# Optimization experiments

Measured on AMD Instinct MI355X. Metric: run time of the kernel, lower is better.

## Reference

```python
import jax, jax.numpy as jnp
import numpy as np
from jax.scipy.special import gammaln, logsumexp

S, K, O, H = 64, 16, 32, 30   # state_dim, act_dim, obs_dim, horizon
T, N = 200, 512               # seq len, batch
EPS = 1e-6
LOG2PI = float(np.log(2.0 * np.pi))
NUM_PARAMS = S * O * 2 + K * S * S + S + S + 1


def setup_inputs() -> dict:
    key = jax.random.key(0)
    k1, k2, k3 = jax.random.split(key, 3)
    o = jax.random.normal(k1, (T, N, O), dtype=jnp.float32)
    a = jax.random.randint(k2, (T, N), 0, K)
    theta = jax.random.normal(k3, (N, NUM_PARAMS), dtype=jnp.float32)
    return {"o": o, "a": a, "theta": theta}


def _transform_params(theta):
    sizes = [S * O * 2, K * S * S, S, S, 1]
    idx = np.cumsum(sizes)[:-1]
    tA, tB, tC, tD, ttau = jnp.split(theta, idx, axis=-1)
    A_mean, A_lv = jnp.split(tA, 2, axis=-1)
    A_mean = A_mean.reshape(-1, S, O)
    A_std = jax.nn.softplus(A_lv.reshape(-1, S, O)) + EPS  # rectify
    B = jax.nn.softmax(tB.reshape(-1, K, S, S), axis=-1)
    C = jax.nn.softmax(tC.reshape(-1, 1, S), axis=-1)
    D = jax.nn.softmax(tD.reshape(-1, S), axis=-1)
    tau = jax.nn.sigmoid(ttau) * (2.0 * H) + 1.0  # [N,1]
    return A_mean, A_std, B, C, D, tau


def reference(o, a, theta):
    A_mean, A_std, B, C, D, tau = _transform_params(theta)

    # --- negative expected free energy reward: r[n,k,i] ---
    ent = jnp.sum(0.5 + 0.5 * LOG2PI + jnp.log(A_std), axis=-1)          # Normal entropy, [N,S]
    kl = jnp.sum(B * (jnp.log(B + EPS) - jnp.log(C[:, None] + EPS)), -1)  # KL(B || C), [N,K,S]
    eh = jnp.einsum('nkij,nj->nki', B, ent)
    r = -kl - eh

    # --- finite-horizon value iteration: q [H,N,K,S] ---
    def vi_step(qt, _):
        v = logsumexp(qt, axis=-2)                    # [N,S]
        qn = r + jnp.einsum('nkij,nj->nki', B, v)
        return qn, qn
    _, q_rest = jax.lax.scan(vi_step, r, None, length=H - 1)
    q = jnp.concatenate([r[None], q_rest], axis=0)

    # --- truncated poisson horizon weights: pdf [N,H] ---
    hh = jnp.arange(H, dtype=jnp.float32)
    logp_h = hh[None, :] * jnp.log(tau) - tau - gammaln(hh + 1.0)[None, :]
    pdf = jnp.exp(logp_h)
    pdf = pdf / jnp.sum(pdf, axis=-1, keepdims=True)

    batch_idx = jnp.arange(N)

    def time_step(b, inp):
        o_t, a_t = inp
        # policy from current belief
        qb = jnp.einsum('ni,hnki->hnk', b, q)
        pi_h = jax.nn.softmax(qb, axis=-1)
        pi_t = jnp.einsum('hnk,nh->nk', pi_h, pdf)
        # belief update
        B_a = B[batch_idx, a_t]                       # [N,S,S]
        s = jnp.einsum('nij,ni->nj', B_a, b)
        logp_s = jnp.log(s + EPS)
        lp = -0.5 * ((o_t[:, None, :] - A_mean) / A_std) ** 2 \
             - jnp.log(A_std) - 0.5 * LOG2PI          # [N,S,O]
        joint = logp_s + jnp.sum(lp, axis=-1)         # [N,S]
        b_next = jax.nn.softmax(joint, axis=-1)
        logp_o = logsumexp(joint, axis=-1)
        return b_next, (pi_t, b, logp_o)

    _, (pi, b_seq, logp_o) = jax.lax.scan(time_step, D, (o, a))
    return pi, b_seq, logp_o
```

## Files before the change

### kernel.cpp

```cpp
#include <hip/hip_runtime.h>
#include <hip/hip_bf16.h>
#include <math.h>

#define SDIM 64
#define KDIM 16
#define ODIM 32
#define HDIM 30
#define TDIM 200
#define NDIM 512
#define NP 69761
#define EPSV 1e-6f
#define LOG2PIF 1.8378770664093453f

__device__ __forceinline__ float softplusf(float x) {
    return (x > 0.f) ? x + log1pf(expf(-x)) : log1pf(expf(x));
}
__device__ __forceinline__ float wave_max64(float v) {
#pragma unroll
    for (int off = 32; off; off >>= 1) v = fmaxf(v, __shfl_xor(v, off, 64));
    return v;
}
__device__ __forceinline__ float wave_sum64(float v) {
#pragma unroll
    for (int off = 32; off; off >>= 1) v += __shfl_xor(v, off, 64);
    return v;
}
__device__ __forceinline__ void bar_lds() {
    asm volatile("s_waitcnt lgkmcnt(0)\n\ts_barrier" ::: "memory");
}

__global__ __launch_bounds__(256) void transform_kernel(
    const float* __restrict__ theta, float* __restrict__ invstd,
    float* __restrict__ c0, float* __restrict__ ent,
    float* __restrict__ logC, float* __restrict__ Dws,
    float* __restrict__ pdfws)
{
    __shared__ float ls[SDIM * 33];
    const int n = blockIdx.x, tid = threadIdx.x;
    const float* thn = theta + (size_t)n * NP;

    for (int idx = tid; idx < SDIM * ODIM; idx += 256) {
        float x = thn[2048 + idx];
        float sp = softplusf(x) + EPSV;
        invstd[(size_t)n * SDIM * ODIM + idx] = 1.f / sp;
        int s = idx >> 5, oo = idx & 31;
        ls[s * 33 + oo] = logf(sp);
    }
    __syncthreads();

    const int wave = tid >> 6, lane = tid & 63;
    if (wave == 0) {
        float sum = 0.f;
#pragma unroll
        for (int oo = 0; oo < ODIM; ++oo) sum += ls[lane * 33 + oo];
        c0[n * SDIM + lane]  = -sum - 16.f * LOG2PIF;
        ent[n * SDIM + lane] =  sum + 32.f * (0.5f + 0.5f * LOG2PIF);
    } else if (wave == 1) {
        float x = thn[69632 + lane];
        float m = wave_max64(x);
        float e = expf(x - m);
        float ssum = wave_sum64(e);
        logC[n * SDIM + lane] = logf(e / ssum + EPSV);
    } else if (wave == 2) {
        float x = thn[69696 + lane];
        float m = wave_max64(x);
        float e = expf(x - m);
        float ssum = wave_sum64(e);
        Dws[n * SDIM + lane] = e / ssum;
    } else {
        float tt = thn[69760];
        float tau = 60.f / (1.f + expf(-tt)) + 1.f;
        float p = 0.f;
        if (lane < HDIM)
            p = expf((float)lane * logf(tau) - tau - lgammaf((float)lane + 1.f));
        float ssum = wave_sum64(p);
        if (lane < HDIM) pdfws[n * HDIM + lane] = p / ssum;
    }
}

__global__ __launch_bounds__(256) void row_stats_kernel(
    const float* __restrict__ theta, const float* __restrict__ logC,
    const float* __restrict__ ent, float* __restrict__ lse,
    float* __restrict__ rws, __hip_bfloat16* __restrict__ bn)
{
    const int gw = blockIdx.x * 4 + (threadIdx.x >> 6);
    const int lane = threadIdx.x & 63;
    const int n = gw >> 10, rl = gw & 1023;
    float x = theta[(size_t)n * NP + 4096 + (size_t)rl * 64 + lane];
    float m = wave_max64(x);
    float e = expf(x - m);
    float ssum = wave_sum64(e);
    float Bj = e / ssum;
    if (bn) {
        const int k = rl >> 6, i = rl & 63;
        __hip_bfloat16 h = __float2bfloat16(Bj);
        unsigned short bits;
        __builtin_memcpy(&bits, &h, 2);
        ((unsigned short*)bn)[(size_t)n * KDIM * SDIM * SDIM
            + (size_t)k * 4096 + (size_t)(i >> 1) * 128 + lane * 2 + (i & 1)] = bits;
    }
    float contrib = Bj * (logf(Bj + EPSV) - logC[n * SDIM + lane] + ent[n * SDIM + lane]);
    contrib = wave_sum64(contrib);
    if (lane == 0) {
        lse[gw] = m + logf(ssum);
        rws[gw] = -contrib;
    }
}

#define BSYM(T_, U_) do {                                                      \
    const int cur_ = (T_) & 1, nxt_ = cur_ ^ 1;                                \
    {                \
        const float4 b0_ = *(const float4*)&b_buf[wave][rbase];                \
        const float4 b1_ = *(const float4*)&b_buf[wave][rbase + 4];            \
        float accA_ = er[0] * b0_.x + er[1] * b0_.y + er[2] * b0_.z + er[3] * b0_.w; \
        float accB_ = er[4] * b1_.x + er[5] * b1_.y + er[6] * b1_.z + er[7] * b1_.w; \
        part_s[cur_][wave][lane] = accA_ + accB_;                              \
    }                                                                          \
    if (wave == 7) out_b[((size_t)(T_) * NDIM + n) * SDIM + lane] = b_buf[7][lane]; \
    if ((T_) + 1 < TDIM && wave < 4) {                 \
        const int ob_ = wave * 8;                                              \
        const float* om_ = &o_s[((T_) + 1) * ODIM + ob_];                      \
        float zz_ = 0.f;                                                       \
        _Pragma("unroll")                                                      \
        for (int j_ = 0; j_ < 8; ++j_) {                                       \
            float z_ = (om_[j_] - mean_s[lane * 33 + ob_ + j_])                \
                     * istd_s[lane * 33 + ob_ + j_];                           \
            zz_ += z_ * z_;                                                    \
        }                                                                      \
        z2p_s[nxt_][wave][lane] = zz_;                                         \
    }                                                                          \
        \
    const float z2_ = z2p_s[cur_][0][lane] + z2p_s[cur_][1][lane]              \
                    + z2p_s[cur_][2][lane] + z2p_s[cur_][3][lane];             \
    const float c_ = c0_r - 0.5f * z2_;                                        \
    const float cm_ = wave_max64(c_);                                          \
    const float ecz_ = __expf(c_ - cm_);                                       \
    if ((T_) + 1 < TDIM) {                        \
        _Pragma("unroll")                                                      \
        for (int m_ = 0; m_ < 4; ++m_) {                                       \
            er[2 * m_]     = __uint_as_float(U_[m_] << 16);                    \
            er[2 * m_ + 1] = __uint_as_float(U_[m_] & 0xffff0000u);            \
        }                                                                      \
    }                                                                          \
    {                                                 \
        const int tl_ = ((T_) + 3 < TDIM) ? (T_) + 3 : TDIM - 1;               \
        const uint* up_ = bnn32 + (size_t)a_s[tl_] * 2048 + (rbase >> 1) * 64 + lane; \
        _Pragma("unroll")                                                      \
        for (int m_ = 0; m_ < 4; ++m_) U_[m_] = up_[m_ * 64];                  \
    }                                                                          \
    bar_lds();                                            \
    {                                   \
        float sv_ = part_s[cur_][0][lane] + part_s[cur_][1][lane]              \
                  + part_s[cur_][2][lane] + part_s[cur_][3][lane]              \
                  + part_s[cur_][4][lane] + part_s[cur_][5][lane]              \
                  + part_s[cur_][6][lane] + part_s[cur_][7][lane];             \
        float u_ = (sv_ + EPSV) * ecz_;                                        \
        float S_ = wave_sum64(u_);                                             \
        b_buf[wave][lane] = u_ / S_;                                           \
        if (wave == 0 && lane == 0)                                            \
            out_lp[(size_t)(T_) * NDIM + n] = cm_ + __logf(S_);                \
    }                                                                          \
} while (0)

__global__ __launch_bounds__(512) void belief_sym_kernel(
    const float* __restrict__ o, const int* __restrict__ a,
    const float* __restrict__ theta, const __hip_bfloat16* __restrict__ bn,
    const float* __restrict__ invstd, const float* __restrict__ c0g,
    const float* __restrict__ Dws,
    float* __restrict__ out_b, float* __restrict__ out_lp)
{
    __shared__ float o_s[TDIM * ODIM];
    __shared__ int   a_s[TDIM];
    __shared__ float mean_s[SDIM * 33];
    __shared__ float istd_s[SDIM * 33];
    __shared__ float c0_sh[SDIM];
    __shared__ __align__(16) float b_buf[8][SDIM];
    __shared__ float part_s[2][8][68];
    __shared__ float z2p_s[2][4][SDIM];

    const int n = blockIdx.x, tid = threadIdx.x;
    const int wave = tid >> 6, lane = tid & 63;
    const int rbase = wave * 8;
    const float* thn = theta + (size_t)n * NP;
    const uint* bnn32 = (const uint*)(bn + (size_t)n * KDIM * SDIM * SDIM);

    for (int idx = tid; idx < TDIM * ODIM; idx += 512)
        o_s[idx] = o[((size_t)(idx >> 5) * NDIM + n) * ODIM + (idx & 31)];
    if (tid < TDIM) a_s[tid] = a[tid * NDIM + n];
    for (int idx = tid; idx < SDIM * ODIM; idx += 512) {
        int s = idx >> 5, oo = idx & 31;
        mean_s[s * 33 + oo] = thn[idx];
        istd_s[s * 33 + oo] = invstd[(size_t)n * SDIM * ODIM + idx];
    }
    if (tid < SDIM) c0_sh[tid] = c0g[n * SDIM + tid];
    b_buf[wave][lane] = Dws[n * SDIM + lane];
    __syncthreads();

    const float c0_r = c0_sh[lane];

    float er[8];
    uint u0[4], u1[4];
    {
        const uint* p0 = bnn32 + (size_t)a_s[0] * 2048 + (rbase >> 1) * 64 + lane;
#pragma unroll
        for (int m = 0; m < 4; ++m) u0[m] = p0[m * 64];
#pragma unroll
        for (int m = 0; m < 4; ++m) {
            er[2 * m]     = __uint_as_float(u0[m] << 16);
            er[2 * m + 1] = __uint_as_float(u0[m] & 0xffff0000u);
        }
        const uint* p1 = bnn32 + (size_t)a_s[1] * 2048 + (rbase >> 1) * 64 + lane;
#pragma unroll
        for (int m = 0; m < 4; ++m) u0[m] = p1[m * 64];
        const uint* p2 = bnn32 + (size_t)a_s[2] * 2048 + (rbase >> 1) * 64 + lane;
#pragma unroll
        for (int m = 0; m < 4; ++m) u1[m] = p2[m * 64];
        if (wave < 4) {
            const int ob = wave * 8;
            const float* om = &o_s[ob];
            float zz = 0.f;
#pragma unroll
            for (int j = 0; j < 8; ++j) {
                float z = (om[j] - mean_s[lane * 33 + ob + j]) * istd_s[lane * 33 + ob + j];
                zz += z * z;
            }
            z2p_s[0][wave][lane] = zz;
        }
    }
    __syncthreads();

#pragma unroll 1
    for (int t = 0; t < TDIM; t += 2) {
        BSYM(t, u0);
        BSYM(t + 1, u1);
    }
}

#define Z2PART(TT_, BUF_) do {                                                 \
    const int ob_ = (wave - 1) * 8;                                            \
    const float* om_ = &o_s[(TT_) * ODIM + ob_];                               \
    float zz_ = 0.f;                                                           \
    _Pragma("unroll")                                                          \
    for (int j_ = 0; j_ < 8; ++j_) {                                           \
        float z_ = (om_[j_] - mean_s[lane * 33 + ob_ + j_])                    \
                 * istd_s[lane * 33 + ob_ + j_];                               \
        zz_ += z_ * z_;                                                        \
    }                                                                          \
    z2p_s[BUF_][wave - 1][lane] = zz_;                                         \
} while (0)

#define BSTEP(T_, RAW_) do {                                                   \
    const int cur_ = (T_) & 1, nxt_ = cur_ ^ 1;                                \
    if (wave >= 1) {                                                           \
        float acc_ = 0.f;                                                      \
        _Pragma("unroll")                                                      \
        for (int ii = 0; ii < 10; ++ii)                                        \
            if (ii < nrow) acc_ += er[ii] * b_s[cur_][rbase + ii];             \
        part_s[wave - 1][lane] = acc_;                                         \
        if (wave == 6) out_b[((size_t)(T_) * NDIM + n) * SDIM + lane] = b_s[cur_][lane]; \
    }                                                                          \
    bar_lds();                                                                 \
    if (wave == 0) {                                                           \
        float sv_ = part_s[0][lane] + part_s[1][lane] + part_s[2][lane]        \
                  + part_s[3][lane] + part_s[4][lane] + part_s[5][lane]        \
                  + part_s[6][lane];                                           \
        float z2_ = z2p_s[cur_][0][lane] + z2p_s[cur_][1][lane]                \
                  + z2p_s[cur_][2][lane] + z2p_s[cur_][3][lane];               \
        float joint_ = __logf(sv_ + EPSV) + c0_s[lane] - 0.5f * z2_;           \
        float m_ = wave_max64(joint_);                                         \
        float e_ = __expf(joint_ - m_);                                        \
        float ss_ = wave_sum64(e_);                                            \
        b_s[nxt_][lane] = e_ / ss_;                                            \
        if (lane == 0) out_lp[(size_t)(T_) * NDIM + n] = m_ + __logf(ss_);     \
    } else {                                                                   \
        if ((T_) + 1 < TDIM) {                                                 \
            const int an_ = a_s[(T_) + 1];                                     \
            const float* ln_ = lseA + an_ * SDIM;                              \
            _Pragma("unroll")                                                  \
            for (int ii = 0; ii < 10; ++ii)                                    \
                if (ii < nrow) er[ii] = __expf(RAW_[ii] - ln_[rbase + ii]);    \
            if (wave <= 4) Z2PART((T_) + 1, nxt_);                             \
        }                                                                      \
        const int tl_ = ((T_) + 3 < TDIM) ? (T_) + 3 : TDIM - 1;               \
        const int a3_ = a_s[tl_];                                              \
        const float* X3_ = Xn + (size_t)a3_ * SDIM * SDIM;                     \
        _Pragma("unroll")                                                      \
        for (int ii = 0; ii < 10; ++ii)                                        \
            if (ii < nrow) RAW_[ii] = X3_[(size_t)(rbase + ii) * SDIM + lane]; \
    }                                                                          \
    bar_lds();                                                                 \
} while (0)

__global__ __launch_bounds__(512) void belief_kernel(
    const float* __restrict__ o, const int* __restrict__ a,
    const float* __restrict__ theta, const float* __restrict__ lse,
    const float* __restrict__ invstd, const float* __restrict__ c0g,
    const float* __restrict__ Dws,
    float* __restrict__ out_b, float* __restrict__ out_lp)
{
    __shared__ float o_s[TDIM * ODIM];
    __shared__ int   a_s[TDIM];
    __shared__ float mean_s[SDIM * 33];
    __shared__ float istd_s[SDIM * 33];
    __shared__ float lseA[KDIM * SDIM];
    __shared__ float c0_s[SDIM];
    __shared__ float b_s[2][SDIM];
    __shared__ float part_s[7][68];
    __shared__ float z2p_s[2][4][SDIM];

    const int n = blockIdx.x, tid = threadIdx.x;
    const int wave = tid >> 6, lane = tid & 63;
    const float* thn = theta + (size_t)n * NP;
    const float* Xn  = thn + 4096;

    for (int idx = tid; idx < TDIM * ODIM; idx += 512)
        o_s[idx] = o[((size_t)(idx >> 5) * NDIM + n) * ODIM + (idx & 31)];
    if (tid < TDIM) a_s[tid] = a[tid * NDIM + n];
    for (int idx = tid; idx < SDIM * ODIM; idx += 512) {
        int s = idx >> 5, oo = idx & 31;
        mean_s[s * 33 + oo] = thn[idx];
        istd_s[s * 33 + oo] = invstd[(size_t)n * SDIM * ODIM + idx];
    }
    for (int idx = tid; idx < KDIM * SDIM; idx += 512)
        lseA[idx] = lse[(size_t)n * KDIM * SDIM + idx];
    if (tid < SDIM) { c0_s[tid] = c0g[n * SDIM + tid]; b_s[0][tid] = Dws[n * SDIM + tid]; }
    __syncthreads();

    const int rbase = (wave >= 1) ? (wave - 1) * 10 : 0;
    const int nrow  = (wave >= 1) ? ((SDIM - rbase) < 10 ? (SDIM - rbase) : 10) : 0;

    float er[10], raw0[10], raw1[10];
    if (wave >= 1) {
        const int a0 = a_s[0];
        const float* X0 = Xn + (size_t)a0 * SDIM * SDIM;
        const float* l0 = lseA + a0 * SDIM;
#pragma unroll
        for (int ii = 0; ii < 10; ++ii)
            if (ii < nrow) er[ii] = __expf(X0[(size_t)(rbase + ii) * SDIM + lane] - l0[rbase + ii]);
        const int a1 = a_s[1];
        const float* X1 = Xn + (size_t)a1 * SDIM * SDIM;
#pragma unroll
        for (int ii = 0; ii < 10; ++ii)
            if (ii < nrow) raw0[ii] = X1[(size_t)(rbase + ii) * SDIM + lane];
        const int a2 = a_s[2];
        const float* X2 = Xn + (size_t)a2 * SDIM * SDIM;
#pragma unroll
        for (int ii = 0; ii < 10; ++ii)
            if (ii < nrow) raw1[ii] = X2[(size_t)(rbase + ii) * SDIM + lane];
        if (wave <= 4) Z2PART(0, 0);
    }
    __syncthreads();

#pragma unroll 1
    for (int t = 0; t < TDIM; t += 2) {
        BSTEP(t, raw0);
        BSTEP(t + 1, raw1);
    }
}

__global__ __launch_bounds__(512) void vi_kernel(
    const float* __restrict__ theta, const float* __restrict__ lse,
    const float* __restrict__ rws, float* __restrict__ q_ws)
{
    __shared__ float q_lds[KDIM * 68];
    __shared__ __align__(16) float v_lds[68];
    const int n = blockIdx.x, tid = threadIdx.x;
    const float* Xn = theta + (size_t)n * NP + 4096;

    const float l0  = lse[(size_t)n * 1024 + tid];
    const float l1  = lse[(size_t)n * 1024 + 512 + tid];
    const float rr0 = rws[(size_t)n * 1024 + tid];
    const float rr1 = rws[(size_t)n * 1024 + 512 + tid];

    float4 er0[16], er1[16];
    {
        const float* X0 = Xn + (size_t)tid * 64;
        const float* X1 = Xn + (size_t)(512 + tid) * 64;
#pragma unroll
        for (int j = 0; j < 16; ++j) {
            float4 x = *(const float4*)(X0 + j * 4);
            er0[j] = make_float4(__expf(x.x - l0), __expf(x.y - l0),
                                 __expf(x.z - l0), __expf(x.w - l0));
            float4 y = *(const float4*)(X1 + j * 4);
            er1[j] = make_float4(__expf(y.x - l1), __expf(y.y - l1),
                                 __expf(y.z - l1), __expf(y.w - l1));
        }
    }

    float qr0 = rr0, qr1 = rr1;
    float* qw = q_ws + (size_t)n * HDIM * 1024;
    const int kq0 = tid >> 6, iq = tid & 63;
    qw[tid] = qr0;
    qw[512 + tid] = qr1;
    q_lds[kq0 * 68 + iq] = qr0;
    q_lds[(8 + kq0) * 68 + iq] = qr1;
    __syncthreads();

#pragma unroll 1
    for (int h = 1; h < HDIM; ++h) {
        if (tid < 64) {
            float m = -1e30f;
#pragma unroll
            for (int k = 0; k < KDIM; ++k) m = fmaxf(m, q_lds[k * 68 + tid]);
            float s = 0.f;
#pragma unroll
            for (int k = 0; k < KDIM; ++k) s += __expf(q_lds[k * 68 + tid] - m);
            v_lds[tid] = m + __logf(s);
        }
        bar_lds();
        float a0x = 0.f, a0y = 0.f, a0z = 0.f, a0w = 0.f;
        float a1x = 0.f, a1y = 0.f, a1z = 0.f, a1w = 0.f;
#pragma unroll
        for (int jq = 0; jq < 16; ++jq) {
            const float4 v4 = *(const float4*)&v_lds[jq * 4];
            a0x += er0[jq].x * v4.x; a0y += er0[jq].y * v4.y;
            a0z += er0[jq].z * v4.z; a0w += er0[jq].w * v4.w;
            a1x += er1[jq].x * v4.x; a1y += er1[jq].y * v4.y;
            a1z += er1[jq].z * v4.z; a1w += er1[jq].w * v4.w;
        }
        qr0 = rr0 + ((a0x + a0y) + (a0z + a0w));
        qr1 = rr1 + ((a1x + a1y) + (a1z + a1w));
        qw[(size_t)h * 1024 + tid] = qr0;
        qw[(size_t)h * 1024 + 512 + tid] = qr1;
        q_lds[kq0 * 68 + iq] = qr0;
        q_lds[(8 + kq0) * 68 + iq] = qr1;
        bar_lds();
    }
}

__global__ __launch_bounds__(512, 1) void policy_bc_kernel(
    const float* __restrict__ q_ws, const float* __restrict__ out_b_g,
    const float* __restrict__ pdfg, float* __restrict__ out_pi)
{
    __shared__ __align__(16) float b_all[TDIM * SDIM];
    __shared__ float part[2][2][8][16];
    __shared__ float pdf_s[32];

    const int n = blockIdx.x, tid = threadIdx.x;
    const int w = tid >> 6, lane = tid & 63;
    const int hl = lane >> 4, kk = lane & 15;
    const int hown = w * 4 + hl;
    const float* qn = q_ws + (size_t)n * HDIM * 1024;

    for (int idx = tid; idx < TDIM * 16; idx += 512) {
        const int t = idx >> 4, jq = idx & 15;
        *(float4*)&b_all[t * SDIM + jq * 4] =
            *(const float4*)&out_b_g[((size_t)t * NDIM + n) * SDIM + jq * 4];
    }
    if (tid < 32) pdf_s[tid] = (tid < HDIM) ? pdfg[n * HDIM + tid] : 0.f;

    float4 qrow[16];
    if (hown < HDIM) {
#pragma unroll
        for (int jq = 0; jq < 16; ++jq)
            qrow[jq] = *(const float4*)&qn[(size_t)hown * 1024 + kk * 64 + jq * 4];
    } else {
#pragma unroll
        for (int jq = 0; jq < 16; ++jq)
            qrow[jq] = make_float4(0.f, 0.f, 0.f, 0.f);
    }
    __syncthreads();
    const float pdfh = pdf_s[hown];

#define PVAL(T_, OUTV_) do {                                                   \
    const float* br_ = &b_all[(T_) * SDIM];                                    \
    float ax_ = 0.f, ay_ = 0.f, az_ = 0.f, aw_ = 0.f;                          \
    _Pragma("unroll")                                                          \
    for (int jq_ = 0; jq_ < 16; ++jq_) {                                       \
        const float4 b4_ = *(const float4*)&br_[jq_ * 4];                      \
        ax_ += qrow[jq_].x * b4_.x; ay_ += qrow[jq_].y * b4_.y;                \
        az_ += qrow[jq_].z * b4_.z; aw_ += qrow[jq_].w * b4_.w;                \
    }                                                                          \
    float acc_ = (ax_ + ay_) + (az_ + aw_);                                    \
    float m_ = acc_;                                                           \
    m_ = fmaxf(m_, __shfl_xor(m_, 1, 64));                                     \
    m_ = fmaxf(m_, __shfl_xor(m_, 2, 64));                                     \
    m_ = fmaxf(m_, __shfl_xor(m_, 4, 64));                                     \
    m_ = fmaxf(m_, __shfl_xor(m_, 8, 64));                                     \
    float e_ = __expf(acc_ - m_);                                              \
    float S_ = e_;                                                             \
    S_ += __shfl_xor(S_, 1, 64);                                               \
    S_ += __shfl_xor(S_, 2, 64);                                               \
    S_ += __shfl_xor(S_, 4, 64);                                               \
    S_ += __shfl_xor(S_, 8, 64);                                               \
    float v_ = pdfh * e_ / S_;                                                 \
    v_ += __shfl_xor(v_, 16, 64);                                              \
    v_ += __shfl_xor(v_, 32, 64);                                              \
    OUTV_ = v_;                                                                \
} while (0)

#pragma unroll 1
    for (int t0 = 0; t0 < TDIM; t0 += 2) {
        const int buf = (t0 >> 1) & 1;
        float v0, v1;
        PVAL(t0, v0);
        PVAL(t0 + 1, v1);
        if (lane < 16) {
            part[buf][0][w][lane] = v0;
            part[buf][1][w][lane] = v1;
        }
        bar_lds();
        if (w < 2 && lane < 16) {
            float s8 = 0.f;
#pragma unroll
            for (int ww = 0; ww < 8; ++ww) s8 += part[buf][w][ww][lane];
            out_pi[((size_t)(t0 + w) * NDIM + n) * KDIM + lane] = s8;
        }
    }
#undef PVAL
}

__global__ __launch_bounds__(512) void vi_policy_kernel(
    const float* __restrict__ theta, const float* __restrict__ lse,
    const float* __restrict__ rws, const float* __restrict__ pdfg,
    const float* __restrict__ out_b_g, float* __restrict__ out_pi)
{
    __shared__ __align__(16) float q_s[HDIM * KDIM * 68];
    __shared__ float r_s[KDIM * SDIM];
    __shared__ float lse_s[KDIM * SDIM];
    __shared__ __align__(16) float v_s[SDIM];
    __shared__ __align__(16) float b_lds[64 * 68];
    __shared__ float pdf_s[32];

    const int n = blockIdx.x, tid = threadIdx.x;
    const int wave = tid >> 6, lane = tid & 63;
    const int sub = lane & 15, rq = lane >> 4;
    const float* Xn = theta + (size_t)n * NP + 4096;

    for (int idx = tid; idx < KDIM * SDIM; idx += 512) {
        r_s[idx]   = rws[(size_t)n * KDIM * SDIM + idx];
        lse_s[idx] = lse[(size_t)n * KDIM * SDIM + idx];
    }
    if (tid < HDIM) pdf_s[tid] = pdfg[n * HDIM + tid];
    __syncthreads();

    for (int idx = tid; idx < KDIM * SDIM; idx += 512)
        q_s[(idx >> 6) * 68 + (idx & 63)] = r_s[idx];

    float4 breg[32];
#pragma unroll
    for (int it = 0; it < 32; ++it) {
        const int row = it * 32 + wave * 4 + rq;
        const float* xr = Xn + (size_t)row * SDIM + sub * 4;
        const float l = lse_s[row];
        breg[it] = make_float4(__expf(xr[0] - l), __expf(xr[1] - l),
                               __expf(xr[2] - l), __expf(xr[3] - l));
    }
    bar_lds();

#pragma unroll 1
    for (int h = 1; h < HDIM; ++h) {
        if (tid < SDIM) {
            const int base = (h - 1) * KDIM;
            float m = -1e30f;
#pragma unroll
            for (int k = 0; k < KDIM; ++k) m = fmaxf(m, q_s[(base + k) * 68 + tid]);
            float ssum = 0.f;
#pragma unroll
            for (int k = 0; k < KDIM; ++k) ssum += __expf(q_s[(base + k) * 68 + tid] - m);
            v_s[tid] = m + __logf(ssum);
        }
        bar_lds();
        const float4 v4 = *(const float4*)&v_s[sub * 4];
#pragma unroll
        for (int it = 0; it < 32; ++it) {
            const int row = it * 32 + wave * 4 + rq;
            float acc = breg[it].x * v4.x + breg[it].y * v4.y
                      + breg[it].z * v4.z + breg[it].w * v4.w;
            acc += __shfl_xor(acc, 1, 64);
            acc += __shfl_xor(acc, 2, 64);
            acc += __shfl_xor(acc, 4, 64);
            acc += __shfl_xor(acc, 8, 64);
            if (sub == 0)
                q_s[(h * KDIM + (row >> 6)) * 68 + (row & 63)] = r_s[row] + acc;
        }
        bar_lds();
    }

    const int tc = tid >> 4, kk = tid & 15;
#pragma unroll 1
    for (int t0 = 0; t0 < TDIM; t0 += 64) {
        const int nt = (TDIM - t0) < 64 ? (TDIM - t0) : 64;
        for (int idx = tid; idx < nt * 16; idx += 512) {
            const int row = idx >> 4, jq = idx & 15;
            *(float4*)&b_lds[row * 68 + jq * 4] =
                *(const float4*)&out_b_g[(((size_t)(t0 + row)) * NDIM + n) * SDIM + jq * 4];
        }
        bar_lds();
        const bool vA = tc < nt, vB = (tc + 32) < nt;
        float4 bqA[16], bqB[16];
        if (vA) {
#pragma unroll
            for (int jq = 0; jq < 16; ++jq)
                bqA[jq] = *(const float4*)&b_lds[tc * 68 + jq * 4];
        }
        if (vB) {
#pragma unroll
            for (int jq = 0; jq < 16; ++jq)
                bqB[jq] = *(const float4*)&b_lds[(tc + 32) * 68 + jq * 4];
        }
        float pikA = 0.f, pikB = 0.f;
#pragma unroll 1
        for (int h = 0; h < HDIM; ++h) {
            const float* qr = &q_s[(h * KDIM + kk) * 68];
            float aA = 0.f, aB = 0.f;
#pragma unroll
            for (int jq = 0; jq < 16; ++jq) {
                const float4 qv = *(const float4*)&qr[jq * 4];
                if (vA) aA += qv.x * bqA[jq].x + qv.y * bqA[jq].y
                            + qv.z * bqA[jq].z + qv.w * bqA[jq].w;
                if (vB) aB += qv.x * bqB[jq].x + qv.y * bqB[jq].y
                            + qv.z * bqB[jq].z + qv.w * bqB[jq].w;
            }
            float mA = aA, mB = aB;
            mA = fmaxf(mA, __shfl_xor(mA, 1, 64));
            mA = fmaxf(mA, __shfl_xor(mA, 2, 64));
            mA = fmaxf(mA, __shfl_xor(mA, 4, 64));
            mA = fmaxf(mA, __shfl_xor(mA, 8, 64));
            mB = fmaxf(mB, __shfl_xor(mB, 1, 64));
            mB = fmaxf(mB, __shfl_xor(mB, 2, 64));
            mB = fmaxf(mB, __shfl_xor(mB, 4, 64));
            mB = fmaxf(mB, __shfl_xor(mB, 8, 64));
            float eA = __expf(aA - mA), eB = __expf(aB - mB);
            float SA = eA, SB = eB;
            SA += __shfl_xor(SA, 1, 64);
            SA += __shfl_xor(SA, 2, 64);
            SA += __shfl_xor(SA, 4, 64);
            SA += __shfl_xor(SA, 8, 64);
            SB += __shfl_xor(SB, 1, 64);
            SB += __shfl_xor(SB, 2, 64);
            SB += __shfl_xor(SB, 4, 64);
            SB += __shfl_xor(SB, 8, 64);
            const float ph = pdf_s[h];
            pikA += ph * eA / SA;
            pikB += ph * eB / SB;
        }
        if (vA) out_pi[(((size_t)(t0 + tc)) * NDIM + n) * KDIM + kk] = pikA;
        if (vB) out_pi[(((size_t)(t0 + 32 + tc)) * NDIM + n) * KDIM + kk] = pikB;
        bar_lds();
    }
}

extern "C" void kernel_launch(void* const* d_in, const int* in_sizes, int n_in,
                              void* d_out, int out_size, void* d_ws, size_t ws_size,
                              hipStream_t stream) {
    (void)in_sizes; (void)n_in; (void)out_size;
    const float* o     = (const float*)d_in[0];
    const int*   a     = (const int*)d_in[1];
    const float* theta = (const float*)d_in[2];
    float* out = (float*)d_out;
    float* ws  = (float*)d_ws;

    float* lse    = ws;
    float* rws    = lse    + (size_t)NDIM * KDIM * SDIM;
    float* invstd = rws    + (size_t)NDIM * KDIM * SDIM;
    float* c0     = invstd + (size_t)NDIM * SDIM * ODIM;
    float* ent    = c0     + (size_t)NDIM * SDIM;
    float* logC   = ent    + (size_t)NDIM * SDIM;
    float* Dws    = logC   + (size_t)NDIM * SDIM;
    float* pdfws  = Dws    + (size_t)NDIM * SDIM;
    float* q_ws   = pdfws  + (size_t)NDIM * HDIM;
    __hip_bfloat16* bn = (__hip_bfloat16*)(q_ws + (size_t)NDIM * HDIM * KDIM * SDIM);

    const size_t f_base = (size_t)NDIM * KDIM * SDIM * 2
                        + (size_t)NDIM * SDIM * ODIM
                        + (size_t)NDIM * SDIM * 4
                        + (size_t)NDIM * HDIM;
    const size_t f_q  = (size_t)NDIM * HDIM * KDIM * SDIM;
    const size_t need2 = (f_base + f_q) * 4;
    const size_t need1 = need2 + (size_t)NDIM * KDIM * SDIM * SDIM * 2;

    float* out_pi = out;
    float* out_b  = out + (size_t)TDIM * NDIM * KDIM;
    float* out_lp = out + (size_t)TDIM * NDIM * KDIM + (size_t)TDIM * NDIM * SDIM;

    transform_kernel<<<NDIM, 256, 0, stream>>>(theta, invstd, c0, ent, logC, Dws, pdfws);

    if (ws_size >= need1) {
        row_stats_kernel<<<(NDIM * KDIM * SDIM) / 4, 256, 0, stream>>>(
            theta, logC, ent, lse, rws, bn);
        belief_sym_kernel<<<NDIM, 512, 0, stream>>>(
            o, a, theta, bn, invstd, c0, Dws, out_b, out_lp);
        vi_kernel<<<NDIM, 512, 0, stream>>>(theta, lse, rws, q_ws);
        policy_bc_kernel<<<NDIM, 512, 0, stream>>>(q_ws, out_b, pdfws, out_pi);
    } else if (ws_size >= need2) {
        row_stats_kernel<<<(NDIM * KDIM * SDIM) / 4, 256, 0, stream>>>(
            theta, logC, ent, lse, rws, (__hip_bfloat16*)nullptr);
        belief_kernel<<<NDIM, 512, 0, stream>>>(
            o, a, theta, lse, invstd, c0, Dws, out_b, out_lp);
        vi_kernel<<<NDIM, 512, 0, stream>>>(theta, lse, rws, q_ws);
        policy_bc_kernel<<<NDIM, 512, 0, stream>>>(q_ws, out_b, pdfws, out_pi);
    } else {
        row_stats_kernel<<<(NDIM * KDIM * SDIM) / 4, 256, 0, stream>>>(
            theta, logC, ent, lse, rws, (__hip_bfloat16*)nullptr);
        belief_kernel<<<NDIM, 512, 0, stream>>>(
            o, a, theta, lse, invstd, c0, Dws, out_b, out_lp);
        vi_policy_kernel<<<NDIM, 512, 0, stream>>>(theta, lse, rws, pdfws, out_b, out_pi);
    }
}
```

Before: 659.0 us.

## Shrink belief kernel to four waves with shuffle broadcast and batch policy steps

```diff
diff --git a/kernel.cpp b/kernel.cpp
--- a/kernel.cpp
+++ b/kernel.cpp
@@ -107,62 +107,59 @@
     }
 }
 
-#define BSYM(T_, U_) do {                                                      \
+#define BS4(T_, U_) do {                                                       \
     const int cur_ = (T_) & 1, nxt_ = cur_ ^ 1;                                \
-    {                \
-        const float4 b0_ = *(const float4*)&b_buf[wave][rbase];                \
-        const float4 b1_ = *(const float4*)&b_buf[wave][rbase + 4];            \
-        float accA_ = er[0] * b0_.x + er[1] * b0_.y + er[2] * b0_.z + er[3] * b0_.w; \
-        float accB_ = er[4] * b1_.x + er[5] * b1_.y + er[6] * b1_.z + er[7] * b1_.w; \
-        part_s[cur_][wave][lane] = accA_ + accB_;                              \
-    }                                                                          \
-    if (wave == 7) out_b[((size_t)(T_) * NDIM + n) * SDIM + lane] = b_buf[7][lane]; \
-    if ((T_) + 1 < TDIM && wave < 4) {                 \
-        const int ob_ = wave * 8;                                              \
-        const float* om_ = &o_s[((T_) + 1) * ODIM + ob_];                      \
+    if (wave == 3) out_b[((size_t)(T_) * NDIM + n) * SDIM + lane] = bval;      \
+    {      \
+        float a0_ = 0.f, a1_ = 0.f, a2_ = 0.f, a3_ = 0.f;                      \
+        _Pragma("unroll")                                                      \
+        for (int j_ = 0; j_ < 4; ++j_) {                                       \
+            a0_ += er[4 * j_ + 0] * __shfl(bval, rbase + 4 * j_ + 0, 64);      \
+            a1_ += er[4 * j_ + 1] * __shfl(bval, rbase + 4 * j_ + 1, 64);      \
+            a2_ += er[4 * j_ + 2] * __shfl(bval, rbase + 4 * j_ + 2, 64);      \
+            a3_ += er[4 * j_ + 3] * __shfl(bval, rbase + 4 * j_ + 3, 64);      \
+        }                                                                      \
+        part_s[cur_][wave][lane] = (a0_ + a1_) + (a2_ + a3_);                  \
+    }                                                                          \
+    if ((T_) + 1 < TDIM) {                             \
+        const float* om_ = &o_s[((T_) + 1) * ODIM + ob];                       \
         float zz_ = 0.f;                                                       \
         _Pragma("unroll")                                                      \
         for (int j_ = 0; j_ < 8; ++j_) {                                       \
-            float z_ = (om_[j_] - mean_s[lane * 33 + ob_ + j_])                \
-                     * istd_s[lane * 33 + ob_ + j_];                           \
+            float z_ = (om_[j_] - mean_r[j_]) * istd_r[j_];                    \
             zz_ += z_ * z_;                                                    \
         }                                                                      \
         z2p_s[nxt_][wave][lane] = zz_;                                         \
     }                                                                          \
-        \
-    const float z2_ = z2p_s[cur_][0][lane] + z2p_s[cur_][1][lane]              \
-                    + z2p_s[cur_][2][lane] + z2p_s[cur_][3][lane];             \
-    const float c_ = c0_r - 0.5f * z2_;                                        \
-    const float cm_ = wave_max64(c_);                                          \
-    const float ecz_ = __expf(c_ - cm_);                                       \
-    if ((T_) + 1 < TDIM) {                        \
-        _Pragma("unroll")                                                      \
-        for (int m_ = 0; m_ < 4; ++m_) {                                       \
-            er[2 * m_]     = __uint_as_float(U_[m_] << 16);                    \
-            er[2 * m_ + 1] = __uint_as_float(U_[m_] & 0xffff0000u);            \
-        }                                                                      \
+    _Pragma("unroll")                             \
+    for (int m_ = 0; m_ < 8; ++m_) {                                           \
+        er[2 * m_]     = __uint_as_float(U_[m_] << 16);                        \
+        er[2 * m_ + 1] = __uint_as_float(U_[m_] & 0xffff0000u);                \
     }                                                                          \
     {                                                 \
         const int tl_ = ((T_) + 3 < TDIM) ? (T_) + 3 : TDIM - 1;               \
         const uint* up_ = bnn32 + (size_t)a_s[tl_] * 2048 + (rbase >> 1) * 64 + lane; \
         _Pragma("unroll")                                                      \
-        for (int m_ = 0; m_ < 4; ++m_) U_[m_] = up_[m_ * 64];                  \
+        for (int m_ = 0; m_ < 8; ++m_) U_[m_] = up_[m_ * 64];                  \
     }                                                                          \
     bar_lds();                                            \
-    {                                   \
+    {            \
         float sv_ = part_s[cur_][0][lane] + part_s[cur_][1][lane]              \
-                  + part_s[cur_][2][lane] + part_s[cur_][3][lane]              \
-                  + part_s[cur_][4][lane] + part_s[cur_][5][lane]              \
-                  + part_s[cur_][6][lane] + part_s[cur_][7][lane];             \
-        float u_ = (sv_ + EPSV) * ecz_;                                        \
+                  + part_s[cur_][2][lane] + part_s[cur_][3][lane];             \
+        float u_ = (sv_ + EPSV) * ecz_cur;                                     \
         float S_ = wave_sum64(u_);                                             \
-        b_buf[wave][lane] = u_ / S_;                                           \
         if (wave == 0 && lane == 0)                                            \
-            out_lp[(size_t)(T_) * NDIM + n] = cm_ + __logf(S_);                \
+            out_lp[(size_t)(T_) * NDIM + n] = cm_cur + __logf(S_);             \
+        bval = u_ / S_;                                                        \
+        float z2n_ = z2p_s[nxt_][0][lane] + z2p_s[nxt_][1][lane]               \
+                   + z2p_s[nxt_][2][lane] + z2p_s[nxt_][3][lane];              \
+        float cn_ = c0_r - 0.5f * z2n_;                                        \
+        cm_cur = wave_max64(cn_);                                              \
+        ecz_cur = __expf(cn_ - cm_cur);                                        \
     }                                                                          \
 } while (0)
 
-__global__ __launch_bounds__(512) void belief_sym_kernel(
+__global__ __launch_bounds__(256) void belief4_kernel(
     const float* __restrict__ o, const int* __restrict__ a,
     const float* __restrict__ theta, const __hip_bfloat16* __restrict__ bn,
     const float* __restrict__ invstd, const float* __restrict__ c0g,
@@ -174,65 +171,77 @@
     __shared__ float mean_s[SDIM * 33];
     __shared__ float istd_s[SDIM * 33];
     __shared__ float c0_sh[SDIM];
-    __shared__ __align__(16) float b_buf[8][SDIM];
-    __shared__ float part_s[2][8][68];
+    __shared__ float part_s[2][4][68];
     __shared__ float z2p_s[2][4][SDIM];
 
     const int n = blockIdx.x, tid = threadIdx.x;
     const int wave = tid >> 6, lane = tid & 63;
-    const int rbase = wave * 8;
+    const int rbase = wave * 16, ob = wave * 8;
     const float* thn = theta + (size_t)n * NP;
     const uint* bnn32 = (const uint*)(bn + (size_t)n * KDIM * SDIM * SDIM);
 
-    for (int idx = tid; idx < TDIM * ODIM; idx += 512)
+    for (int idx = tid; idx < TDIM * ODIM; idx += 256)
         o_s[idx] = o[((size_t)(idx >> 5) * NDIM + n) * ODIM + (idx & 31)];
     if (tid < TDIM) a_s[tid] = a[tid * NDIM + n];
-    for (int idx = tid; idx < SDIM * ODIM; idx += 512) {
+    for (int idx = tid; idx < SDIM * ODIM; idx += 256) {
         int s = idx >> 5, oo = idx & 31;
         mean_s[s * 33 + oo] = thn[idx];
         istd_s[s * 33 + oo] = invstd[(size_t)n * SDIM * ODIM + idx];
     }
     if (tid < SDIM) c0_sh[tid] = c0g[n * SDIM + tid];
-    b_buf[wave][lane] = Dws[n * SDIM + lane];
     __syncthreads();
 
     const float c0_r = c0_sh[lane];
-
-    float er[8];
-    uint u0[4], u1[4];
+    float bval = Dws[n * SDIM + lane];
+    float mean_r[8], istd_r[8];
+#pragma unroll
+    for (int j = 0; j < 8; ++j) {
+        mean_r[j] = mean_s[lane * 33 + ob + j];
+        istd_r[j] = istd_s[lane * 33 + ob + j];
+    }
+
+    float er[16];
+    uint u0[8], u1[8];
     {
         const uint* p0 = bnn32 + (size_t)a_s[0] * 2048 + (rbase >> 1) * 64 + lane;
 #pragma unroll
-        for (int m = 0; m < 4; ++m) u0[m] = p0[m * 64];
-#pragma unroll
-        for (int m = 0; m < 4; ++m) {
+        for (int m = 0; m < 8; ++m) u0[m] = p0[m * 64];
+#pragma unroll
+        for (int m = 0; m < 8; ++m) {
             er[2 * m]     = __uint_as_float(u0[m] << 16);
             er[2 * m + 1] = __uint_as_float(u0[m] & 0xffff0000u);
         }
         const uint* p1 = bnn32 + (size_t)a_s[1] * 2048 + (rbase >> 1) * 64 + lane;
 #pragma unroll
-        for (int m = 0; m < 4; ++m) u0[m] = p1[m * 64];
+        for (int m = 0; m < 8; ++m) u0[m] = p1[m * 64];
         const uint* p2 = bnn32 + (size_t)a_s[2] * 2048 + (rbase >> 1) * 64 + lane;
 #pragma unroll
-        for (int m = 0; m < 4; ++m) u1[m] = p2[m * 64];
-        if (wave < 4) {
-            const int ob = wave * 8;
-            const float* om = &o_s[ob];
-            float zz = 0.f;
-#pragma unroll
-            for (int j = 0; j < 8; ++j) {
-                float z = (om[j] - mean_s[lane * 33 + ob + j]) * istd_s[lane * 33 + ob + j];
-                zz += z * z;
-            }
-            z2p_s[0][wave][lane] = zz;
-        }
+        for (int m = 0; m < 8; ++m) u1[m] = p2[m * 64];
+    }
+    {
+        const float* om = &o_s[ob];
+        float zz = 0.f;
+#pragma unroll
+        for (int j = 0; j < 8; ++j) {
+            float z = (om[j] - mean_r[j]) * istd_r[j];
+            zz += z * z;
+        }
+        z2p_s[0][wave][lane] = zz;
     }
     __syncthreads();
+    float ecz_cur, cm_cur;
+    {
+        float z2 = z2p_s[0][0][lane] + z2p_s[0][1][lane]
+                 + z2p_s[0][2][lane] + z2p_s[0][3][lane];
+        float c = c0_r - 0.5f * z2;
+        cm_cur = wave_max64(c);
+        ecz_cur = __expf(c - cm_cur);
+    }
 
 #pragma unroll 1
     for (int t = 0; t < TDIM; t += 2) {
-        BSYM(t, u0);
-        BSYM(t + 1, u1);
+        BS4(t, u0);
+        BS4(t + 1, u1);
     }
 }
 
@@ -433,7 +442,7 @@
     const float* __restrict__ pdfg, float* __restrict__ out_pi)
 {
     __shared__ __align__(16) float b_all[TDIM * SDIM];
-    __shared__ float part[2][2][8][16];
+    __shared__ float part[2][8][8][17];
     __shared__ float pdf_s[32];
 
     const int n = blockIdx.x, tid = threadIdx.x;
@@ -490,17 +499,19 @@
 } while (0)
 
 #pragma unroll 1
-    for (int t0 = 0; t0 < TDIM; t0 += 2) {
-        const int buf = (t0 >> 1) & 1;
-        float v0, v1;
-        PVAL(t0, v0);
-        PVAL(t0 + 1, v1);
+    for (int t0 = 0; t0 < TDIM; t0 += 8) {
+        const int buf = (t0 >> 3) & 1;
+        float v0, v1, v2, v3, v4, v5, v6, v7;
+        PVAL(t0 + 0, v0); PVAL(t0 + 1, v1); PVAL(t0 + 2, v2); PVAL(t0 + 3, v3);
+        PVAL(t0 + 4, v4); PVAL(t0 + 5, v5); PVAL(t0 + 6, v6); PVAL(t0 + 7, v7);
         if (lane < 16) {
-            part[buf][0][w][lane] = v0;
-            part[buf][1][w][lane] = v1;
+            part[buf][0][w][lane] = v0; part[buf][1][w][lane] = v1;
+            part[buf][2][w][lane] = v2; part[buf][3][w][lane] = v3;
+            part[buf][4][w][lane] = v4; part[buf][5][w][lane] = v5;
+            part[buf][6][w][lane] = v6; part[buf][7][w][lane] = v7;
         }
         bar_lds();
-        if (w < 2 && lane < 16) {
+        if (lane < 16) {
             float s8 = 0.f;
 #pragma unroll
             for (int ww = 0; ww < 8; ++ww) s8 += part[buf][w][ww][lane];
@@ -679,7 +690,7 @@
     if (ws_size >= need1) {
         row_stats_kernel<<<(NDIM * KDIM * SDIM) / 4, 256, 0, stream>>>(
             theta, logC, ent, lse, rws, bn);
-        belief_sym_kernel<<<NDIM, 512, 0, stream>>>(
+        belief4_kernel<<<NDIM, 256, 0, stream>>>(
             o, a, theta, bn, invstd, c0, Dws, out_b, out_lp);
         vi_kernel<<<NDIM, 512, 0, stream>>>(theta, lse, rws, q_ws);
         policy_bc_kernel<<<NDIM, 512, 0, stream>>>(q_ws, out_b, pdfws, out_pi);
```

New measurement: 643.4 us. 2.4% less time.
